# Performance work log

Measured on AMD Instinct MI355X. Metric: run time of the kernel, lower is better.

Reference implementation:

```python
import jax, jax.numpy as jnp
import numpy as np

UNITS = 32
BACKBONE = 64

def lecun_tanh(x):
    return 1.7159 * jnp.tanh(0.666 * x)

def setup_inputs() -> dict:
    key = jax.random.key(0)
    ks = jax.random.split(key, 6)
    B, C, T, H, W = 4, 16, 32, 64, 64
    scale_b = 1.0 / np.sqrt(C + UNITS)
    scale_h = 1.0 / np.sqrt(BACKBONE)
    return {
        "x": jax.random.normal(ks[0], (B, C, T, H, W), jnp.float32),
        "Wb": jax.random.normal(ks[1], (BACKBONE, C + UNITS), jnp.float32) * scale_b,
        "bb": jnp.zeros((BACKBONE,), jnp.float32),
        "Wff1": jax.random.normal(ks[2], (UNITS, BACKBONE), jnp.float32) * scale_h,
        "bff1": jnp.zeros((UNITS,), jnp.float32),
        "Wff2": jax.random.normal(ks[3], (UNITS, BACKBONE), jnp.float32) * scale_h,
        "bff2": jnp.zeros((UNITS,), jnp.float32),
        "Wta": jax.random.normal(ks[4], (UNITS, BACKBONE), jnp.float32) * scale_h,
        "bta": jnp.zeros((UNITS,), jnp.float32),
        "Wtb": jax.random.normal(ks[5], (UNITS, BACKBONE), jnp.float32) * scale_h,
        "btb": jnp.zeros((UNITS,), jnp.float32),
    }

def reference(x, Wb, bb, Wff1, bff1, Wff2, bff2, Wta, bta, Wtb, btb):
    # x: (B, C, T, H, W) -> time-major (T, B, C, H, W) for the scan
    xs = jnp.transpose(x, (2, 0, 1, 3, 4))
    B, C, H, W = x.shape[0], x.shape[1], x.shape[3], x.shape[4]
    h0 = jnp.zeros((B, UNITS, H, W), x.dtype)
    ts = jnp.asarray(1.0, x.dtype)  # no timespans provided -> ts = 1.0

    def head(z, Wh, bh):  # channel-wise (1x1) linear: (B,K,H,W) -> (B,U,H,W)
        return jnp.einsum('bkhw,uk->buhw', z, Wh) + bh[None, :, None, None]

    def step(h, xt):
        z = jnp.concatenate([xt, h], axis=1)  # (B, C+U, H, W)
        z = lecun_tanh(jnp.einsum('bchw,kc->bkhw', z, Wb) + bb[None, :, None, None])
        ff1 = jnp.tanh(head(z, Wff1, bff1))
        ff2 = jnp.tanh(head(z, Wff2, bff2))
        t_a = head(z, Wta, bta)
        t_b = head(z, Wtb, btb)
        t_interp = jax.nn.sigmoid(t_a * ts + t_b)
        h_new = ff1 * (1.0 - t_interp) + t_interp * ff2
        return h_new, h_new

    _, ys = jax.lax.scan(step, h0, xs)  # ys: (T, B, U, H, W)
    # stack along dim=1 (batch_first) then permute(0,2,1,3,4) -> (B, U, T, H, W)
    return jnp.transpose(ys, (1, 2, 0, 3, 4))
```

## Files before the change

kernel.cpp:

```cpp
#include <hip/hip_runtime.h>
#include <hip/hip_bf16.h>


#define CIN      16
#define UNITS    32
#define BACKBONE 64
#define CZ       48
#define TSTEPS   32
#define HW       4096
#define NPIX     16
#define NTHREADS 256

typedef __attribute__((ext_vector_type(8))) short  short8;
typedef __attribute__((ext_vector_type(8))) __bf16 bf16x8;
typedef __attribute__((ext_vector_type(4))) float  float4v;
typedef __attribute__((ext_vector_type(4))) unsigned int uint4v;
typedef __attribute__((ext_vector_type(2))) unsigned int uint2v;

#define BAR_LDS() asm volatile("s_waitcnt lgkmcnt(0)\n\ts_barrier" ::: "memory")

__device__ __forceinline__ unsigned short bf16_rne(float f) {
    unsigned u = __float_as_uint(f);
    return (unsigned short)((u + 0x7FFFu + ((u >> 16) & 1u)) >> 16);
}
__device__ __forceinline__ float bf16_tof(unsigned short h) {
    return __uint_as_float(((unsigned)h) << 16);
}
__device__ __forceinline__ unsigned cvt_pk_bf16(float lo, float hi) {
    unsigned r;
    asm("v_cvt_pk_bf16_f32 %0, %1, %2" : "=v"(r) : "v"(lo), "v"(hi));
    return r;
}

#if __has_builtin(__builtin_amdgcn_exp2f)
#define EXP2F(x) __builtin_amdgcn_exp2f(x)
#else
#define EXP2F(x) __expf(0.69314718056f * (x))
#endif
#if __has_builtin(__builtin_amdgcn_rcpf)
#define RCPF(x) __builtin_amdgcn_rcpf(x)
#else
#define RCPF(x) __fdividef(1.0f, (x))
#endif

__device__ __forceinline__ float lecun_tanh_f(float v) {
    float e = EXP2F(1.92166925f * v);
    return fmaf(-3.4318f, RCPF(e + 1.0f), 1.7159f);
}
__device__ __forceinline__ float tanh_f(float v) {
    float e = EXP2F(2.88539008f * v);
    return fmaf(-2.0f, RCPF(e + 1.0f), 1.0f);
}
__device__ __forceinline__ float sigmoid_f(float v) {
    float e = EXP2F(-1.44269504f * v);
    return RCPF(1.0f + e);
}
__device__ __forceinline__ float4v mfma16(bf16x8 a, bf16x8 b, float4v c) {
    return __builtin_amdgcn_mfma_f32_16x16x32_bf16(a, b, c, 0, 0, 0);
}
__device__ __forceinline__ void split8(const float* v, bf16x8& hi, bf16x8& lo) {
    short8 sh, sl;
    #pragma unroll
    for (int j = 0; j < 8; ++j) {
        unsigned short h = bf16_rne(v[j]);
        sh[j] = (short)h;
        sl[j] = (short)bf16_rne(v[j] - bf16_tof(h));
    }
    hi = __builtin_bit_cast(bf16x8, sh);
    lo = __builtin_bit_cast(bf16x8, sl);
}

__global__ __launch_bounds__(NTHREADS, 4)
void cfc_mfma_kernel(const float* __restrict__ x,   const float* __restrict__ Wb,
                     const float* __restrict__ bb,
                     const float* __restrict__ Wff1, const float* __restrict__ bff1,
                     const float* __restrict__ Wff2, const float* __restrict__ bff2,
                     const float* __restrict__ Wta,  const float* __restrict__ bta,
                     const float* __restrict__ Wtb,  const float* __restrict__ btb,
                     float* __restrict__ out)
{
    __shared__ unsigned abuf[4][64][2];
    __shared__ unsigned hbuf[4][64];

    const int tid  = threadIdx.x;
    const int w    = tid >> 6;
    const int lane = tid & 63;
    const int ln   = lane & 15;
    const int lq   = lane >> 4;

    const int gpix = blockIdx.x * NPIX;
    const int b    = gpix >> 12;
    const int pinb = gpix & 4095;
    const int px   = pinb + ln;

    bf16x8 A1hi[2], A1lo[2];
    #pragma unroll
    for (int kt = 0; kt < 2; ++kt) {
        float v[8];
        #pragma unroll
        for (int j = 0; j < 8; ++j) {
            int c = kt * 32 + lq * 8 + j;
            v[j] = (c < CZ) ? Wb[(w * 16 + ln) * CZ + c] : 0.0f;
        }
        split8(v, A1hi[kt], A1lo[kt]);
    }
    float bbias[4];
    #pragma unroll
    for (int r = 0; r < 4; ++r) bbias[r] = bb[w * 16 + lq * 4 + r];

    const int head = ln & 3;
    const float* Whp = (head == 0) ? Wff1 : (head == 1) ? Wff2 : (head == 2) ? Wta : Wtb;
    const int urow = (((ln >> 2) + 2) & 3) * 8;
    bf16x8 Ah_hi[2][2], Ah_lo[2][2];
    #pragma unroll
    for (int i2 = 0; i2 < 2; ++i2) {
        const int u = urow + 2 * w + i2;
        #pragma unroll
        for (int kt = 0; kt < 2; ++kt) {
            float v[8];
            #pragma unroll
            for (int j = 0; j < 8; ++j) {
                int n = 32 * kt + (j >> 2) * 16 + lq * 4 + (j & 3);
                v[j] = Whp[u * BACKBONE + n];
            }
            split8(v, Ah_hi[i2][kt], Ah_lo[i2][kt]);
        }
    }
    const int ub = ((lq + 2) & 3) * 8;
    float hbias[2][4];
    #pragma unroll
    for (int i2 = 0; i2 < 2; ++i2) {
        int u2 = ub + 2 * w + i2;
        hbias[i2][0] = bff1[u2]; hbias[i2][1] = bff2[u2];
        hbias[i2][2] = bta[u2];  hbias[i2][3] = btb[u2];
    }

    const int cb = (lq & 1) * 8;
    unsigned xo[8], oo[2];
    #pragma unroll
    for (int j = 0; j < 8; ++j)
        xo[j] = (unsigned)(((b * CIN + cb + j) * TSTEPS) * HW + px);
    #pragma unroll
    for (int i2 = 0; i2 < 2; ++i2)
        oo[i2] = (unsigned)(((b * UNITS + ub + 2 * w + i2) * TSTEPS) * HW + px);

    hbuf[w][lane] = 0u;
    float xa[8], xb2[8];
    #pragma unroll
    for (int j = 0; j < 8; ++j) xa[j] = x[xo[j]];
    unsigned toff = 0;
    BAR_LDS();

    auto step = [&](int t, float (&xc)[8], float (&xn)[8]) {
        const unsigned tn = toff + ((t < TSTEPS - 1) ? (unsigned)HW : 0u);
        #pragma unroll
        for (int j = 0; j < 8; ++j) xn[j] = x[xo[j] + tn];

        unsigned hpk[4];
        #pragma unroll
        for (int p = 0; p < 4; ++p) hpk[p] = hbuf[p][lane];

        unsigned xpk[4];
        #pragma unroll
        for (int p = 0; p < 4; ++p) xpk[p] = cvt_pk_bf16(xc[2 * p], xc[2 * p + 1]);
        const bool xl = (lq < 2);
        unsigned z0u[4], z1u[4];
        #pragma unroll
        for (int p = 0; p < 4; ++p) {
            z0u[p] = xl ? xpk[p] : hpk[p];
            z1u[p] = xl ? hpk[p] : 0u;
        }
        uint4v zv0 = {z0u[0], z0u[1], z0u[2], z0u[3]};
        uint4v zv1 = {z1u[0], z1u[1], z1u[2], z1u[3]};
        bf16x8 Z0 = __builtin_bit_cast(bf16x8, zv0);
        bf16x8 Z1 = __builtin_bit_cast(bf16x8, zv1);

        float4v a = {bbias[0], bbias[1], bbias[2], bbias[3]};
        a = mfma16(A1hi[0], Z0, a);
        a = mfma16(A1lo[0], Z0, a);
        a = mfma16(A1hi[1], Z1, a);
        a = mfma16(A1lo[1], Z1, a);

        {
            float g0 = lecun_tanh_f(a[0]);
            float g1 = lecun_tanh_f(a[1]);
            float g2 = lecun_tanh_f(a[2]);
            float g3 = lecun_tanh_f(a[3]);
            uint2v d = {cvt_pk_bf16(g0, g1), cvt_pk_bf16(g2, g3)};
            *(uint2v*)&abuf[w][lane][0] = d;
        }
        BAR_LDS();

        uint2v a01 = *(const uint2v*)&abuf[0][lane][0];
        uint2v a23 = *(const uint2v*)&abuf[1][lane][0];
        uint2v a45 = *(const uint2v*)&abuf[2][lane][0];
        uint2v a67 = *(const uint2v*)&abuf[3][lane][0];
        uint4v w0 = {a01[0], a01[1], a23[0], a23[1]};
        uint4v w1 = {a45[0], a45[1], a67[0], a67[1]};
        bf16x8 A2[2] = {__builtin_bit_cast(bf16x8, w0), __builtin_bit_cast(bf16x8, w1)};

        float hn[2];
        #pragma unroll
        for (int i2 = 0; i2 < 2; ++i2) {
            float4v c = {hbias[i2][0], hbias[i2][1], hbias[i2][2], hbias[i2][3]};
            c = mfma16(Ah_hi[i2][0], A2[0], c);
            c = mfma16(Ah_lo[i2][0], A2[0], c);
            c = mfma16(Ah_hi[i2][1], A2[1], c);
            c = mfma16(Ah_lo[i2][1], A2[1], c);
            float f1 = tanh_f(c[0]);
            float f2 = tanh_f(c[1]);
            float ti = sigmoid_f(c[2] + c[3]);
            float h  = fmaf(ti, f2 - f1, f1);
            out[oo[i2] + toff] = h;
            hn[i2] = h;
        }
        hbuf[w][lane] = cvt_pk_bf16(hn[0], hn[1]);
        BAR_LDS();
        toff += (unsigned)HW;
    };

    #pragma unroll 1
    for (int t = 0; t < TSTEPS; t += 2) {
        step(t,     xa,  xb2);
        step(t + 1, xb2, xa);
    }
}

extern "C" void kernel_launch(void* const* d_in, const int* in_sizes, int n_in,
                              void* d_out, int out_size, void* d_ws, size_t ws_size,
                              hipStream_t stream) {
    dim3 grid(4 * HW / NPIX);
    cfc_mfma_kernel<<<grid, NTHREADS, 0, stream>>>(
        (const float*)d_in[0], (const float*)d_in[1], (const float*)d_in[2],
        (const float*)d_in[3], (const float*)d_in[4], (const float*)d_in[5],
        (const float*)d_in[6], (const float*)d_in[7], (const float*)d_in[8],
        (const float*)d_in[9], (const float*)d_in[10],
        (float*)d_out);
}
```

Before: 160.2 us.

## Split recurrent step across eight waves with LDS-staged operands and partial sums

Doubles the block to 512 threads. The hi and lo bf16 halves of the backbone matmul now run on separate wave groups, whose partial sums are combined through a new LDS buffer. Each wave computes one head row instead of two. The x and h operands are staged into a swizzled LDS z-buffer, so each wave reads them with vector loads instead of building them from registers. This cuts the MFMA and activation work on each wave's critical path in the latency-bound time loop, at the cost of an extra barrier per step and more LDS traffic.

```diff
diff --git a/kernel.cpp b/kernel.cpp
--- a/kernel.cpp
+++ b/kernel.cpp
@@ -9,11 +9,12 @@
 #define TSTEPS   32
 #define HW       4096
 #define NPIX     16
-#define NTHREADS 256
+#define NTHREADS 512
 
 typedef __attribute__((ext_vector_type(8))) short  short8;
 typedef __attribute__((ext_vector_type(8))) __bf16 bf16x8;
 typedef __attribute__((ext_vector_type(4))) float  float4v;
+typedef __attribute__((ext_vector_type(2))) float  float2v;
 typedef __attribute__((ext_vector_type(4))) unsigned int uint4v;
 typedef __attribute__((ext_vector_type(2))) unsigned int uint2v;
 
@@ -70,7 +71,7 @@
     lo = __builtin_bit_cast(bf16x8, sl);
 }
 
-__global__ __launch_bounds__(NTHREADS, 4)
+__global__ __launch_bounds__(NTHREADS, 8)
 void cfc_mfma_kernel(const float* __restrict__ x,   const float* __restrict__ Wb,
                      const float* __restrict__ bb,
                      const float* __restrict__ Wff1, const float* __restrict__ bff1,
@@ -79,8 +80,9 @@
                      const float* __restrict__ Wtb,  const float* __restrict__ btb,
                      float* __restrict__ out)
 {
-    __shared__ unsigned abuf[4][64][2];
-    __shared__ unsigned hbuf[4][64];
+    __shared__ __align__(16) unsigned zbuf[64 * 8];
+    __shared__ __align__(16) unsigned abuf[64 * 8];
+    __shared__ __align__(16) float    pbuf[8][64][2];
 
     const int tid  = threadIdx.x;
     const int w    = tid >> 6;
@@ -91,138 +93,136 @@
     const int gpix = blockIdx.x * NPIX;
     const int b    = gpix >> 12;
     const int pinb = gpix & 4095;
-    const int px   = pinb + ln;
-
-    bf16x8 A1hi[2], A1lo[2];
+
+    const int mt = w & 3;
+    const int hf = w >> 2;
+
+    bf16x8 A1[2];
     #pragma unroll
     for (int kt = 0; kt < 2; ++kt) {
         float v[8];
         #pragma unroll
         for (int j = 0; j < 8; ++j) {
             int c = kt * 32 + lq * 8 + j;
-            v[j] = (c < CZ) ? Wb[(w * 16 + ln) * CZ + c] : 0.0f;
+            v[j] = (c < CZ) ? Wb[(mt * 16 + ln) * CZ + c] : 0.0f;
         }
-        split8(v, A1hi[kt], A1lo[kt]);
+        bf16x8 hi, lo;
+        split8(v, hi, lo);
+        A1[kt] = hf ? lo : hi;
     }
     float bbias[4];
     #pragma unroll
-    for (int r = 0; r < 4; ++r) bbias[r] = bb[w * 16 + lq * 4 + r];
+    for (int r = 0; r < 4; ++r) bbias[r] = bb[mt * 16 + lq * 4 + r];
 
     const int head = ln & 3;
     const float* Whp = (head == 0) ? Wff1 : (head == 1) ? Wff2 : (head == 2) ? Wta : Wtb;
     const int urow = (((ln >> 2) + 2) & 3) * 8;
-    bf16x8 Ah_hi[2][2], Ah_lo[2][2];
-    #pragma unroll
-    for (int i2 = 0; i2 < 2; ++i2) {
-        const int u = urow + 2 * w + i2;
+    bf16x8 Ah_hi[2], Ah_lo[2];
+    #pragma unroll
+    for (int kt = 0; kt < 2; ++kt) {
+        float v[8];
         #pragma unroll
-        for (int kt = 0; kt < 2; ++kt) {
-            float v[8];
-            #pragma unroll
-            for (int j = 0; j < 8; ++j) {
-                int n = 32 * kt + (j >> 2) * 16 + lq * 4 + (j & 3);
-                v[j] = Whp[u * BACKBONE + n];
-            }
-            split8(v, Ah_hi[i2][kt], Ah_lo[i2][kt]);
+        for (int j = 0; j < 8; ++j) {
+            int n = 32 * kt + (j >> 2) * 16 + lq * 4 + (j & 3);
+            v[j] = Whp[(urow + w) * BACKBONE + n];
         }
+        split8(v, Ah_hi[kt], Ah_lo[kt]);
     }
     const int ub = ((lq + 2) & 3) * 8;
-    float hbias[2][4];
-    #pragma unroll
-    for (int i2 = 0; i2 < 2; ++i2) {
-        int u2 = ub + 2 * w + i2;
-        hbias[i2][0] = bff1[u2]; hbias[i2][1] = bff2[u2];
-        hbias[i2][2] = bta[u2];  hbias[i2][3] = btb[u2];
-    }
-
-    const int cb = (lq & 1) * 8;
-    unsigned xo[8], oo[2];
-    #pragma unroll
-    for (int j = 0; j < 8; ++j)
-        xo[j] = (unsigned)(((b * CIN + cb + j) * TSTEPS) * HW + px);
-    #pragma unroll
-    for (int i2 = 0; i2 < 2; ++i2)
-        oo[i2] = (unsigned)(((b * UNITS + ub + 2 * w + i2) * TSTEPS) * HW + px);
-
-    hbuf[w][lane] = 0u;
-    float xa[8], xb2[8];
-    #pragma unroll
-    for (int j = 0; j < 8; ++j) xa[j] = x[xo[j]];
+    const int u2 = ub + w;
+    float hbias[4];
+    hbias[0] = bff1[u2]; hbias[1] = bff2[u2];
+    hbias[2] = bta[u2];  hbias[3] = btb[u2];
+
+    const int zr0 = lane * 8 + (lane & 1) * 4;
+    const int zr1 = lane * 8 + ((lane & 1) ^ 1) * 4;
+    const int d_h  = ((lq < 2) ? 4 : 0) + (w >> 1);
+    const int h_us = (lane * 8 + (((d_h >> 2) ^ (lane & 1)) << 2) + (d_h & 3)) * 2 + (w & 1);
+    const int ai   = mt * 2 + hf;
+    const int a_wr = lane * 8 + (((ai >> 2) ^ (lane & 1)) << 2) + (ai & 3);
+
+    const int xch  = w * 4 + lq;
+    const int cl   = (xch >> 3) * 16 + ln;
+    const int d_x  = (xch & 7) >> 1;
+    const int x_us = (cl * 8 + ((cl & 1) << 2) + d_x) * 2 + (xch & 1);
+    const unsigned xidx = ((unsigned)(b * CIN + xch) * TSTEPS) * HW + (unsigned)(pinb + ln);
+
+    const unsigned oo = ((unsigned)(b * UNITS + u2) * TSTEPS) * HW + (unsigned)(pinb + ln);
+
+    zbuf[tid] = 0u;
+    float xfa = 0.0f, xfb = 0.0f;
+    if (w < 4) {
+        xfa = x[xidx];
+        xfb = x[xidx + HW];
+    }
+    __syncthreads();
+    if (w < 4) {
+        unsigned p0 = cvt_pk_bf16(xfa, xfa);
+        ((unsigned short*)zbuf)[x_us] = (unsigned short)p0;
+    }
+    __syncthreads();
+
     unsigned toff = 0;
-    BAR_LDS();
-
-    auto step = [&](int t, float (&xc)[8], float (&xn)[8]) {
-        const unsigned tn = toff + ((t < TSTEPS - 1) ? (unsigned)HW : 0u);
-        #pragma unroll
-        for (int j = 0; j < 8; ++j) xn[j] = x[xo[j] + tn];
-
-        unsigned hpk[4];
-        #pragma unroll
-        for (int p = 0; p < 4; ++p) hpk[p] = hbuf[p][lane];
-
-        unsigned xpk[4];
-        #pragma unroll
-        for (int p = 0; p < 4; ++p) xpk[p] = cvt_pk_bf16(xc[2 * p], xc[2 * p + 1]);
-        const bool xl = (lq < 2);
-        unsigned z0u[4], z1u[4];
-        #pragma unroll
-        for (int p = 0; p < 4; ++p) {
-            z0u[p] = xl ? xpk[p] : hpk[p];
-            z1u[p] = xl ? hpk[p] : 0u;
-        }
-        uint4v zv0 = {z0u[0], z0u[1], z0u[2], z0u[3]};
-        uint4v zv1 = {z1u[0], z1u[1], z1u[2], z1u[3]};
+
+    auto step = [&](int t, float xcur, float& xnext) {
+        uint4v zv0 = *(const uint4v*)&zbuf[zr0];
+        uint4v zv1 = *(const uint4v*)&zbuf[zr1];
         bf16x8 Z0 = __builtin_bit_cast(bf16x8, zv0);
         bf16x8 Z1 = __builtin_bit_cast(bf16x8, zv1);
 
-        float4v a = {bbias[0], bbias[1], bbias[2], bbias[3]};
-        a = mfma16(A1hi[0], Z0, a);
-        a = mfma16(A1lo[0], Z0, a);
-        a = mfma16(A1hi[1], Z1, a);
-        a = mfma16(A1lo[1], Z1, a);
-
-        {
-            float g0 = lecun_tanh_f(a[0]);
-            float g1 = lecun_tanh_f(a[1]);
-            float g2 = lecun_tanh_f(a[2]);
-            float g3 = lecun_tanh_f(a[3]);
-            uint2v d = {cvt_pk_bf16(g0, g1), cvt_pk_bf16(g2, g3)};
-            *(uint2v*)&abuf[w][lane][0] = d;
+        float4v a;
+        if (hf == 0) { a[0] = bbias[0]; a[1] = bbias[1]; a[2] = bbias[2]; a[3] = bbias[3]; }
+        else         { a[0] = 0.f; a[1] = 0.f; a[2] = 0.f; a[3] = 0.f; }
+        a = mfma16(A1[0], Z0, a);
+        a = mfma16(A1[1], Z1, a);
+
+        const int cp = hf ? 0 : 2;
+        float2v pw = {a[cp], a[cp + 1]};
+        *(float2v*)&pbuf[w][lane][0] = pw;
+        BAR_LDS();
+
+        if (w < 4) {
+            const int tl = (t + 2 < TSTEPS) ? t + 2 : TSTEPS - 1;
+            xnext = x[xidx + (unsigned)tl * HW];
+            unsigned px = cvt_pk_bf16(xcur, xcur);
+            ((unsigned short*)zbuf)[x_us] = (unsigned short)px;
         }
+
+        float2v pp = *(const float2v*)&pbuf[w ^ 4][lane][0];
+        const int sp = hf ? 2 : 0;
+        float s0 = a[sp]     + pp[0];
+        float s1 = a[sp + 1] + pp[1];
+        float g0 = lecun_tanh_f(s0);
+        float g1 = lecun_tanh_f(s1);
+        abuf[a_wr] = cvt_pk_bf16(g0, g1);
         BAR_LDS();
 
-        uint2v a01 = *(const uint2v*)&abuf[0][lane][0];
-        uint2v a23 = *(const uint2v*)&abuf[1][lane][0];
-        uint2v a45 = *(const uint2v*)&abuf[2][lane][0];
-        uint2v a67 = *(const uint2v*)&abuf[3][lane][0];
-        uint4v w0 = {a01[0], a01[1], a23[0], a23[1]};
-        uint4v w1 = {a45[0], a45[1], a67[0], a67[1]};
-        bf16x8 A2[2] = {__builtin_bit_cast(bf16x8, w0), __builtin_bit_cast(bf16x8, w1)};
-
-        float hn[2];
-        #pragma unroll
-        for (int i2 = 0; i2 < 2; ++i2) {
-            float4v c = {hbias[i2][0], hbias[i2][1], hbias[i2][2], hbias[i2][3]};
-            c = mfma16(Ah_hi[i2][0], A2[0], c);
-            c = mfma16(Ah_lo[i2][0], A2[0], c);
-            c = mfma16(Ah_hi[i2][1], A2[1], c);
-            c = mfma16(Ah_lo[i2][1], A2[1], c);
-            float f1 = tanh_f(c[0]);
-            float f2 = tanh_f(c[1]);
-            float ti = sigmoid_f(c[2] + c[3]);
-            float h  = fmaf(ti, f2 - f1, f1);
-            out[oo[i2] + toff] = h;
-            hn[i2] = h;
-        }
-        hbuf[w][lane] = cvt_pk_bf16(hn[0], hn[1]);
+        uint4v w0 = *(const uint4v*)&abuf[zr0];
+        uint4v w1 = *(const uint4v*)&abuf[zr1];
+        bf16x8 A20 = __builtin_bit_cast(bf16x8, w0);
+        bf16x8 A21 = __builtin_bit_cast(bf16x8, w1);
+
+        float4v c;
+        c[0] = hbias[0]; c[1] = hbias[1]; c[2] = hbias[2]; c[3] = hbias[3];
+        c = mfma16(Ah_hi[0], A20, c);
+        c = mfma16(Ah_lo[0], A20, c);
+        c = mfma16(Ah_hi[1], A21, c);
+        c = mfma16(Ah_lo[1], A21, c);
+        float f1 = tanh_f(c[0]);
+        float f2 = tanh_f(c[1]);
+        float ti = sigmoid_f(c[2] + c[3]);
+        float h  = fmaf(ti, f2 - f1, f1);
+        out[oo + toff] = h;
+        unsigned hp = cvt_pk_bf16(h, h);
+        ((unsigned short*)zbuf)[h_us] = (unsigned short)hp;
         BAR_LDS();
         toff += (unsigned)HW;
     };
 
     #pragma unroll 1
     for (int t = 0; t < TSTEPS; t += 2) {
-        step(t,     xa,  xb2);
-        step(t + 1, xb2, xa);
+        step(t,     xfb, xfa);
+        step(t + 1, xfa, xfb);
     }
 }
 
```

Result: slower. 174.4 us (+8.9%).

## Double block to eight waves, splitting backbone and prefetch roles across waves

Applied to the files above, without the earlier changes.

Raises the block to 512 threads. Waves 0-3 compute the backbone MFMA, while waves 4-7 prefetch x two steps ahead and stage it as packed bf16 in LDS. All eight waves then run the head MFMAs, each wave producing one unit instead of two. The aim is to halve the per-wave head work on the serial recurrence critical path and move the x loads off it. The cost is more waves per block competing for the same SIMDs, plus an extra LDS staging buffer and write.

```diff
diff --git a/kernel.cpp b/kernel.cpp
--- a/kernel.cpp
+++ b/kernel.cpp
@@ -9,13 +9,12 @@
 #define TSTEPS   32
 #define HW       4096
 #define NPIX     16
-#define NTHREADS 256
+#define NTHREADS 512
 
 typedef __attribute__((ext_vector_type(8))) short  short8;
 typedef __attribute__((ext_vector_type(8))) __bf16 bf16x8;
 typedef __attribute__((ext_vector_type(4))) float  float4v;
 typedef __attribute__((ext_vector_type(4))) unsigned int uint4v;
-typedef __attribute__((ext_vector_type(2))) unsigned int uint2v;
 
 #define BAR_LDS() asm volatile("s_waitcnt lgkmcnt(0)\n\ts_barrier" ::: "memory")
 
@@ -70,7 +69,7 @@
     lo = __builtin_bit_cast(bf16x8, sl);
 }
 
-__global__ __launch_bounds__(NTHREADS, 4)
+__global__ __launch_bounds__(NTHREADS, 8)
 void cfc_mfma_kernel(const float* __restrict__ x,   const float* __restrict__ Wb,
                      const float* __restrict__ bb,
                      const float* __restrict__ Wff1, const float* __restrict__ bff1,
@@ -79,8 +78,9 @@
                      const float* __restrict__ Wtb,  const float* __restrict__ btb,
                      float* __restrict__ out)
 {
-    __shared__ unsigned abuf[4][64][2];
     __shared__ unsigned hbuf[4][64];
+    __shared__ unsigned abuf[8][64];
+    __shared__ unsigned xbuf[8][16];
 
     const int tid  = threadIdx.x;
     const int w    = tid >> 6;
@@ -91,7 +91,8 @@
     const int gpix = blockIdx.x * NPIX;
     const int b    = gpix >> 12;
     const int pinb = gpix & 4095;
-    const int px   = pinb + ln;
+
+    const int mt = w & 3;
 
     bf16x8 A1hi[2], A1lo[2];
     #pragma unroll
@@ -100,129 +101,130 @@
         #pragma unroll
         for (int j = 0; j < 8; ++j) {
             int c = kt * 32 + lq * 8 + j;
-            v[j] = (c < CZ) ? Wb[(w * 16 + ln) * CZ + c] : 0.0f;
+            v[j] = (c < CZ) ? Wb[(mt * 16 + ln) * CZ + c] : 0.0f;
         }
         split8(v, A1hi[kt], A1lo[kt]);
     }
     float bbias[4];
     #pragma unroll
-    for (int r = 0; r < 4; ++r) bbias[r] = bb[w * 16 + lq * 4 + r];
+    for (int r = 0; r < 4; ++r) bbias[r] = bb[mt * 16 + lq * 4 + r];
 
     const int head = ln & 3;
     const float* Whp = (head == 0) ? Wff1 : (head == 1) ? Wff2 : (head == 2) ? Wta : Wtb;
     const int urow = (((ln >> 2) + 2) & 3) * 8;
-    bf16x8 Ah_hi[2][2], Ah_lo[2][2];
-    #pragma unroll
-    for (int i2 = 0; i2 < 2; ++i2) {
-        const int u = urow + 2 * w + i2;
-        #pragma unroll
-        for (int kt = 0; kt < 2; ++kt) {
-            float v[8];
+    bf16x8 Ah_hi[2], Ah_lo[2];
+    #pragma unroll
+    for (int kt = 0; kt < 2; ++kt) {
+        float v[8];
+        #pragma unroll
+        for (int j = 0; j < 8; ++j) {
+            int n = 32 * kt + (j >> 2) * 16 + lq * 4 + (j & 3);
+            v[j] = Whp[(urow + w) * BACKBONE + n];
+        }
+        split8(v, Ah_hi[kt], Ah_lo[kt]);
+    }
+    const int ub = ((lq + 2) & 3) * 8;
+    const int u2 = ub + w;
+    float hbias[4];
+    hbias[0] = bff1[u2]; hbias[1] = bff2[u2];
+    hbias[2] = bta[u2];  hbias[3] = btb[u2];
+
+    const int xr = 2 * (w & 3) + (lq & 1);
+    const unsigned xi0 = ((unsigned)(b * CIN + 2 * xr) * TSTEPS) * HW
+                         + (unsigned)(pinb + ln);
+    const unsigned xi1 = xi0 + (unsigned)(TSTEPS * HW);
+
+    const unsigned oo = ((unsigned)(b * UNITS + u2) * TSTEPS) * HW
+                        + (unsigned)(pinb + ln);
+
+    unsigned short* const hwp =
+        (unsigned short*)&hbuf[w >> 1][lane] + (w & 1);
+
+    if (tid < 256) ((unsigned*)hbuf)[tid] = 0u;
+    float c0 = 0.f, c1 = 0.f, n0 = 0.f, n1 = 0.f;
+    if (w >= 4 && lq < 2) {
+        float a0 = x[xi0], a1 = x[xi1];
+        xbuf[xr][ln] = cvt_pk_bf16(a0, a1);
+        c0 = x[xi0 + HW]; c1 = x[xi1 + HW];
+    }
+    __syncthreads();
+
+    unsigned toff = 0;
+
+    auto step = [&](int t, float cx0, float cx1, float& nx0, float& nx1) {
+        if (w < 4) {
+            unsigned hpk[4], xpk[4];
             #pragma unroll
-            for (int j = 0; j < 8; ++j) {
-                int n = 32 * kt + (j >> 2) * 16 + lq * 4 + (j & 3);
-                v[j] = Whp[u * BACKBONE + n];
+            for (int p = 0; p < 4; ++p) hpk[p] = hbuf[p][lane];
+            #pragma unroll
+            for (int p = 0; p < 4; ++p) xpk[p] = xbuf[(lq & 1) * 4 + p][ln];
+
+            const bool xl = (lq < 2);
+            unsigned z0u[4], z1u[4];
+            #pragma unroll
+            for (int p = 0; p < 4; ++p) {
+                z0u[p] = xl ? xpk[p] : hpk[p];
+                z1u[p] = xl ? hpk[p] : 0u;
             }
-            split8(v, Ah_hi[i2][kt], Ah_lo[i2][kt]);
-        }
-    }
-    const int ub = ((lq + 2) & 3) * 8;
-    float hbias[2][4];
-    #pragma unroll
-    for (int i2 = 0; i2 < 2; ++i2) {
-        int u2 = ub + 2 * w + i2;
-        hbias[i2][0] = bff1[u2]; hbias[i2][1] = bff2[u2];
-        hbias[i2][2] = bta[u2];  hbias[i2][3] = btb[u2];
-    }
-
-    const int cb = (lq & 1) * 8;
-    unsigned xo[8], oo[2];
-    #pragma unroll
-    for (int j = 0; j < 8; ++j)
-        xo[j] = (unsigned)(((b * CIN + cb + j) * TSTEPS) * HW + px);
-    #pragma unroll
-    for (int i2 = 0; i2 < 2; ++i2)
-        oo[i2] = (unsigned)(((b * UNITS + ub + 2 * w + i2) * TSTEPS) * HW + px);
-
-    hbuf[w][lane] = 0u;
-    float xa[8], xb2[8];
-    #pragma unroll
-    for (int j = 0; j < 8; ++j) xa[j] = x[xo[j]];
-    unsigned toff = 0;
-    BAR_LDS();
-
-    auto step = [&](int t, float (&xc)[8], float (&xn)[8]) {
-        const unsigned tn = toff + ((t < TSTEPS - 1) ? (unsigned)HW : 0u);
-        #pragma unroll
-        for (int j = 0; j < 8; ++j) xn[j] = x[xo[j] + tn];
-
-        unsigned hpk[4];
-        #pragma unroll
-        for (int p = 0; p < 4; ++p) hpk[p] = hbuf[p][lane];
-
-        unsigned xpk[4];
-        #pragma unroll
-        for (int p = 0; p < 4; ++p) xpk[p] = cvt_pk_bf16(xc[2 * p], xc[2 * p + 1]);
-        const bool xl = (lq < 2);
-        unsigned z0u[4], z1u[4];
-        #pragma unroll
-        for (int p = 0; p < 4; ++p) {
-            z0u[p] = xl ? xpk[p] : hpk[p];
-            z1u[p] = xl ? hpk[p] : 0u;
-        }
-        uint4v zv0 = {z0u[0], z0u[1], z0u[2], z0u[3]};
-        uint4v zv1 = {z1u[0], z1u[1], z1u[2], z1u[3]};
-        bf16x8 Z0 = __builtin_bit_cast(bf16x8, zv0);
-        bf16x8 Z1 = __builtin_bit_cast(bf16x8, zv1);
-
-        float4v a = {bbias[0], bbias[1], bbias[2], bbias[3]};
-        a = mfma16(A1hi[0], Z0, a);
-        a = mfma16(A1lo[0], Z0, a);
-        a = mfma16(A1hi[1], Z1, a);
-        a = mfma16(A1lo[1], Z1, a);
-
-        {
+            uint4v zv0 = {z0u[0], z0u[1], z0u[2], z0u[3]};
+            uint4v zv1 = {z1u[0], z1u[1], z1u[2], z1u[3]};
+            bf16x8 Z0 = __builtin_bit_cast(bf16x8, zv0);
+            bf16x8 Z1 = __builtin_bit_cast(bf16x8, zv1);
+
+            float4v a = {bbias[0], bbias[1], bbias[2], bbias[3]};
+            a = mfma16(A1hi[0], Z0, a);
+            a = mfma16(A1lo[0], Z0, a);
+            a = mfma16(A1hi[1], Z1, a);
+            a = mfma16(A1lo[1], Z1, a);
+
             float g0 = lecun_tanh_f(a[0]);
             float g1 = lecun_tanh_f(a[1]);
             float g2 = lecun_tanh_f(a[2]);
             float g3 = lecun_tanh_f(a[3]);
-            uint2v d = {cvt_pk_bf16(g0, g1), cvt_pk_bf16(g2, g3)};
-            *(uint2v*)&abuf[w][lane][0] = d;
+            abuf[mt * 2 + 0][lane] = cvt_pk_bf16(g0, g1);
+            abuf[mt * 2 + 1][lane] = cvt_pk_bf16(g2, g3);
+        } else {
+            const int tl = (t + 2 < TSTEPS) ? t + 2 : TSTEPS - 1;
+            if (lq < 2) {
+                nx0 = x[xi0 + (unsigned)tl * HW];
+                nx1 = x[xi1 + (unsigned)tl * HW];
+            }
         }
         BAR_LDS();
 
-        uint2v a01 = *(const uint2v*)&abuf[0][lane][0];
-        uint2v a23 = *(const uint2v*)&abuf[1][lane][0];
-        uint2v a45 = *(const uint2v*)&abuf[2][lane][0];
-        uint2v a67 = *(const uint2v*)&abuf[3][lane][0];
-        uint4v w0 = {a01[0], a01[1], a23[0], a23[1]};
-        uint4v w1 = {a45[0], a45[1], a67[0], a67[1]};
-        bf16x8 A2[2] = {__builtin_bit_cast(bf16x8, w0), __builtin_bit_cast(bf16x8, w1)};
-
-        float hn[2];
-        #pragma unroll
-        for (int i2 = 0; i2 < 2; ++i2) {
-            float4v c = {hbias[i2][0], hbias[i2][1], hbias[i2][2], hbias[i2][3]};
-            c = mfma16(Ah_hi[i2][0], A2[0], c);
-            c = mfma16(Ah_lo[i2][0], A2[0], c);
-            c = mfma16(Ah_hi[i2][1], A2[1], c);
-            c = mfma16(Ah_lo[i2][1], A2[1], c);
-            float f1 = tanh_f(c[0]);
-            float f2 = tanh_f(c[1]);
-            float ti = sigmoid_f(c[2] + c[3]);
-            float h  = fmaf(ti, f2 - f1, f1);
-            out[oo[i2] + toff] = h;
-            hn[i2] = h;
-        }
-        hbuf[w][lane] = cvt_pk_bf16(hn[0], hn[1]);
+        if (w >= 4 && lq < 2)
+            xbuf[xr][ln] = cvt_pk_bf16(cx0, cx1);
+
+        unsigned f0[4], f1[4];
+        #pragma unroll
+        for (int d = 0; d < 4; ++d) f0[d] = abuf[d][lane];
+        #pragma unroll
+        for (int d = 0; d < 4; ++d) f1[d] = abuf[4 + d][lane];
+        uint4v w0 = {f0[0], f0[1], f0[2], f0[3]};
+        uint4v w1 = {f1[0], f1[1], f1[2], f1[3]};
+        bf16x8 A20 = __builtin_bit_cast(bf16x8, w0);
+        bf16x8 A21 = __builtin_bit_cast(bf16x8, w1);
+
+        float4v c = {hbias[0], hbias[1], hbias[2], hbias[3]};
+        c = mfma16(Ah_hi[0], A20, c);
+        c = mfma16(Ah_lo[0], A20, c);
+        c = mfma16(Ah_hi[1], A21, c);
+        c = mfma16(Ah_lo[1], A21, c);
+        float f1g = tanh_f(c[0]);
+        float f2g = tanh_f(c[1]);
+        float ti  = sigmoid_f(c[2] + c[3]);
+        float h   = fmaf(ti, f2g - f1g, f1g);
+        out[oo + toff] = h;
+        unsigned hp = cvt_pk_bf16(h, h);
+        *hwp = (unsigned short)hp;
         BAR_LDS();
         toff += (unsigned)HW;
     };
 
     #pragma unroll 1
     for (int t = 0; t < TSTEPS; t += 2) {
-        step(t,     xa,  xb2);
-        step(t + 1, xb2, xa);
+        step(t,     c0, c1, n0, n1);
+        step(t + 1, n0, n1, c0, c1);
     }
 }
 
```

Result: slower. 192.7 us (+20.3%).

## Split backbone GEMM into x-part precomputed ahead and h-part on critical path

Applied to the files above, without the earlier changes.

Splits the backbone matmul into an input-projection part (Wx·x + bias) and a recurrent part (Wh·h). The x contribution for the next step is computed off the critical path, between the barriers, and x loads are prefetched two steps ahead. The recurrent dependency chain then holds only two MFMAs instead of four. The LDS layout for the activation buffer also changes to single-word rows, and the row/unit permutation is simplified. This adds x-projection MFMAs and extra registers for the double-buffered partial sums.

```diff
diff --git a/kernel.cpp b/kernel.cpp
--- a/kernel.cpp
+++ b/kernel.cpp
@@ -15,7 +15,6 @@
 typedef __attribute__((ext_vector_type(8))) __bf16 bf16x8;
 typedef __attribute__((ext_vector_type(4))) float  float4v;
 typedef __attribute__((ext_vector_type(4))) unsigned int uint4v;
-typedef __attribute__((ext_vector_type(2))) unsigned int uint2v;
 
 #define BAR_LDS() asm volatile("s_waitcnt lgkmcnt(0)\n\ts_barrier" ::: "memory")
 
@@ -79,8 +78,8 @@
                      const float* __restrict__ Wtb,  const float* __restrict__ btb,
                      float* __restrict__ out)
 {
-    __shared__ unsigned abuf[4][64][2];
     __shared__ unsigned hbuf[4][64];
+    __shared__ unsigned abuf[8][64];
 
     const int tid  = threadIdx.x;
     const int w    = tid >> 6;
@@ -91,42 +90,46 @@
     const int gpix = blockIdx.x * NPIX;
     const int b    = gpix >> 12;
     const int pinb = gpix & 4095;
-    const int px   = pinb + ln;
-
-    bf16x8 A1hi[2], A1lo[2];
-    #pragma unroll
-    for (int kt = 0; kt < 2; ++kt) {
+    const int mt   = w;
+
+    bf16x8 Whhi, Whlo;
+    {
         float v[8];
         #pragma unroll
-        for (int j = 0; j < 8; ++j) {
-            int c = kt * 32 + lq * 8 + j;
-            v[j] = (c < CZ) ? Wb[(w * 16 + ln) * CZ + c] : 0.0f;
-        }
-        split8(v, A1hi[kt], A1lo[kt]);
+        for (int j = 0; j < 8; ++j)
+            v[j] = Wb[(mt * 16 + ln) * CZ + CIN + lq * 8 + j];
+        split8(v, Whhi, Whlo);
+    }
+    bf16x8 Wxhi, Wxlo;
+    {
+        float v[8];
+        #pragma unroll
+        for (int j = 0; j < 8; ++j)
+            v[j] = (lq < 2) ? Wb[(mt * 16 + ln) * CZ + lq * 8 + j] : 0.0f;
+        split8(v, Wxhi, Wxlo);
     }
     float bbias[4];
     #pragma unroll
-    for (int r = 0; r < 4; ++r) bbias[r] = bb[w * 16 + lq * 4 + r];
+    for (int r = 0; r < 4; ++r) bbias[r] = bb[mt * 16 + lq * 4 + r];
 
     const int head = ln & 3;
     const float* Whp = (head == 0) ? Wff1 : (head == 1) ? Wff2 : (head == 2) ? Wta : Wtb;
-    const int urow = (((ln >> 2) + 2) & 3) * 8;
+    const int urow = (ln >> 2) * 8;
     bf16x8 Ah_hi[2][2], Ah_lo[2][2];
     #pragma unroll
     for (int i2 = 0; i2 < 2; ++i2) {
-        const int u = urow + 2 * w + i2;
         #pragma unroll
         for (int kt = 0; kt < 2; ++kt) {
             float v[8];
             #pragma unroll
             for (int j = 0; j < 8; ++j) {
                 int n = 32 * kt + (j >> 2) * 16 + lq * 4 + (j & 3);
-                v[j] = Whp[u * BACKBONE + n];
+                v[j] = Whp[(urow + 2 * w + i2) * BACKBONE + n];
             }
             split8(v, Ah_hi[i2][kt], Ah_lo[i2][kt]);
         }
     }
-    const int ub = ((lq + 2) & 3) * 8;
+    const int ub = lq * 8;
     float hbias[2][4];
     #pragma unroll
     for (int i2 = 0; i2 < 2; ++i2) {
@@ -135,82 +138,98 @@
         hbias[i2][2] = bta[u2];  hbias[i2][3] = btb[u2];
     }
 
-    const int cb = (lq & 1) * 8;
-    unsigned xo[8], oo[2];
-    #pragma unroll
-    for (int j = 0; j < 8; ++j)
-        xo[j] = (unsigned)(((b * CIN + cb + j) * TSTEPS) * HW + px);
+    unsigned xo[8];
+    #pragma unroll
+    for (int j = 0; j < 8; ++j) {
+        int ch = (lq < 2) ? (lq * 8 + j) : 0;
+        xo[j] = ((unsigned)(b * CIN + ch) * TSTEPS) * HW + (unsigned)(pinb + ln);
+    }
+    unsigned oo[2];
     #pragma unroll
     for (int i2 = 0; i2 < 2; ++i2)
-        oo[i2] = (unsigned)(((b * UNITS + ub + 2 * w + i2) * TSTEPS) * HW + px);
-
-    hbuf[w][lane] = 0u;
-    float xa[8], xb2[8];
-    #pragma unroll
-    for (int j = 0; j < 8; ++j) xa[j] = x[xo[j]];
+        oo[i2] = ((unsigned)(b * UNITS + ub + 2 * w + i2) * TSTEPS) * HW
+                 + (unsigned)(pinb + ln);
+
+    auto packx = [&](const float (&v)[8]) {
+        uint4v u = {cvt_pk_bf16(v[0], v[1]), cvt_pk_bf16(v[2], v[3]),
+                    cvt_pk_bf16(v[4], v[5]), cvt_pk_bf16(v[6], v[7])};
+        return __builtin_bit_cast(bf16x8, u);
+    };
+
+    ((unsigned*)hbuf)[tid] = 0u;
+    float xv0[8] = {0,0,0,0,0,0,0,0}, xv1[8] = {0,0,0,0,0,0,0,0};
+    if (lq < 2) {
+        #pragma unroll
+        for (int j = 0; j < 8; ++j) xv0[j] = x[xo[j]];
+    }
+    float4v xzA, xzB;
+    {
+        bf16x8 X0 = packx(xv0);
+        float4v a = {bbias[0], bbias[1], bbias[2], bbias[3]};
+        a = mfma16(Wxhi, X0, a);
+        a = mfma16(Wxlo, X0, a);
+        xzA = a;
+    }
+    if (lq < 2) {
+        #pragma unroll
+        for (int j = 0; j < 8; ++j) xv1[j] = x[xo[j] + HW];
+    }
+    __syncthreads();
     unsigned toff = 0;
-    BAR_LDS();
-
-    auto step = [&](int t, float (&xc)[8], float (&xn)[8]) {
-        const unsigned tn = toff + ((t < TSTEPS - 1) ? (unsigned)HW : 0u);
-        #pragma unroll
-        for (int j = 0; j < 8; ++j) xn[j] = x[xo[j] + tn];
-
-        unsigned hpk[4];
-        #pragma unroll
-        for (int p = 0; p < 4; ++p) hpk[p] = hbuf[p][lane];
-
-        unsigned xpk[4];
-        #pragma unroll
-        for (int p = 0; p < 4; ++p) xpk[p] = cvt_pk_bf16(xc[2 * p], xc[2 * p + 1]);
-        const bool xl = (lq < 2);
-        unsigned z0u[4], z1u[4];
-        #pragma unroll
-        for (int p = 0; p < 4; ++p) {
-            z0u[p] = xl ? xpk[p] : hpk[p];
-            z1u[p] = xl ? hpk[p] : 0u;
-        }
-        uint4v zv0 = {z0u[0], z0u[1], z0u[2], z0u[3]};
-        uint4v zv1 = {z1u[0], z1u[1], z1u[2], z1u[3]};
-        bf16x8 Z0 = __builtin_bit_cast(bf16x8, zv0);
-        bf16x8 Z1 = __builtin_bit_cast(bf16x8, zv1);
-
-        float4v a = {bbias[0], bbias[1], bbias[2], bbias[3]};
-        a = mfma16(A1hi[0], Z0, a);
-        a = mfma16(A1lo[0], Z0, a);
-        a = mfma16(A1hi[1], Z1, a);
-        a = mfma16(A1lo[1], Z1, a);
+
+    auto step = [&](int t, float4v xzc, float4v& xzn,
+                    float (&xvi)[8], float (&xvp)[8]) {
+        const int tl = (t + 2 < TSTEPS) ? t + 2 : TSTEPS - 1;
+        if (lq < 2) {
+            #pragma unroll
+            for (int j = 0; j < 8; ++j) xvi[j] = x[xo[j] + (unsigned)tl * HW];
+        }
+
+        unsigned h0 = hbuf[0][lane], h1 = hbuf[1][lane];
+        unsigned h2 = hbuf[2][lane], h3 = hbuf[3][lane];
+        uint4v zv = {h0, h1, h2, h3};
+        bf16x8 Z = __builtin_bit_cast(bf16x8, zv);
+        float4v a = xzc;
+        a = mfma16(Whhi, Z, a);
+        a = mfma16(Whlo, Z, a);
+        float g0 = lecun_tanh_f(a[0]);
+        float g1 = lecun_tanh_f(a[1]);
+        float g2 = lecun_tanh_f(a[2]);
+        float g3 = lecun_tanh_f(a[3]);
+        abuf[mt * 2 + 0][lane] = cvt_pk_bf16(g0, g1);
+        abuf[mt * 2 + 1][lane] = cvt_pk_bf16(g2, g3);
+        BAR_LDS();
 
         {
-            float g0 = lecun_tanh_f(a[0]);
-            float g1 = lecun_tanh_f(a[1]);
-            float g2 = lecun_tanh_f(a[2]);
-            float g3 = lecun_tanh_f(a[3]);
-            uint2v d = {cvt_pk_bf16(g0, g1), cvt_pk_bf16(g2, g3)};
-            *(uint2v*)&abuf[w][lane][0] = d;
-        }
-        BAR_LDS();
-
-        uint2v a01 = *(const uint2v*)&abuf[0][lane][0];
-        uint2v a23 = *(const uint2v*)&abuf[1][lane][0];
-        uint2v a45 = *(const uint2v*)&abuf[2][lane][0];
-        uint2v a67 = *(const uint2v*)&abuf[3][lane][0];
-        uint4v w0 = {a01[0], a01[1], a23[0], a23[1]};
-        uint4v w1 = {a45[0], a45[1], a67[0], a67[1]};
-        bf16x8 A2[2] = {__builtin_bit_cast(bf16x8, w0), __builtin_bit_cast(bf16x8, w1)};
+            bf16x8 X = packx(xvp);
+            float4v q = {bbias[0], bbias[1], bbias[2], bbias[3]};
+            q = mfma16(Wxhi, X, q);
+            q = mfma16(Wxlo, X, q);
+            xzn = q;
+        }
+
+        unsigned f0[4], f1[4];
+        #pragma unroll
+        for (int d = 0; d < 4; ++d) f0[d] = abuf[d][lane];
+        #pragma unroll
+        for (int d = 0; d < 4; ++d) f1[d] = abuf[4 + d][lane];
+        uint4v w0 = {f0[0], f0[1], f0[2], f0[3]};
+        uint4v w1 = {f1[0], f1[1], f1[2], f1[3]};
+        bf16x8 A20 = __builtin_bit_cast(bf16x8, w0);
+        bf16x8 A21 = __builtin_bit_cast(bf16x8, w1);
 
         float hn[2];
         #pragma unroll
         for (int i2 = 0; i2 < 2; ++i2) {
             float4v c = {hbias[i2][0], hbias[i2][1], hbias[i2][2], hbias[i2][3]};
-            c = mfma16(Ah_hi[i2][0], A2[0], c);
-            c = mfma16(Ah_lo[i2][0], A2[0], c);
-            c = mfma16(Ah_hi[i2][1], A2[1], c);
-            c = mfma16(Ah_lo[i2][1], A2[1], c);
-            float f1 = tanh_f(c[0]);
-            float f2 = tanh_f(c[1]);
-            float ti = sigmoid_f(c[2] + c[3]);
-            float h  = fmaf(ti, f2 - f1, f1);
+            c = mfma16(Ah_hi[i2][0], A20, c);
+            c = mfma16(Ah_lo[i2][0], A20, c);
+            c = mfma16(Ah_hi[i2][1], A21, c);
+            c = mfma16(Ah_lo[i2][1], A21, c);
+            float f1g = tanh_f(c[0]);
+            float f2g = tanh_f(c[1]);
+            float ti  = sigmoid_f(c[2] + c[3]);
+            float h   = fmaf(ti, f2g - f1g, f1g);
             out[oo[i2] + toff] = h;
             hn[i2] = h;
         }
@@ -221,8 +240,8 @@
 
     #pragma unroll 1
     for (int t = 0; t < TSTEPS; t += 2) {
-        step(t,     xa,  xb2);
-        step(t + 1, xb2, xa);
+        step(t,     xzA, xzB, xv0, xv1);
+        step(t + 1, xzB, xzA, xv1, xv0);
     }
 }
 
```

New measurement: 168.0 us. 1.05x slower.
